# Optimization experiments

Measured on AMD Instinct MI355X. Metric: run time of the kernel, lower is better.

## Reference

```python
import jax, jax.numpy as jnp
import numpy as np

B, S, H, NH = 4, 2048, 512, 8  # batch, seq, hidden, heads
D = H // NH                    # head dim = 64


def setup_inputs() -> dict:
    key = jax.random.key(0)
    ks = jax.random.split(key, 12)
    wscale = 1.0 / np.sqrt(H)
    mk = lambda k, sh: jax.random.normal(k, sh, jnp.float32)
    return {
        "q": mk(ks[0], (B, S, H)),
        "k": mk(ks[1], (B, S, H)),
        "v": mk(ks[2], (B, S, H)),
        "k_b": mk(ks[3], (B, S, H)),
        "mask": jax.random.randint(ks[4], (B, S), 0, 2).astype(jnp.int32),
        "Wq": mk(ks[5], (H, H)) * wscale, "bq": jnp.zeros((H,), jnp.float32),
        "Wk": mk(ks[6], (H, H)) * wscale, "bk": jnp.zeros((H,), jnp.float32),
        "Wv": mk(ks[7], (H, H)) * wscale, "bv": jnp.zeros((H,), jnp.float32),
        "Wkb": mk(ks[8], (H, H)) * wscale, "bkb": jnp.zeros((H,), jnp.float32),
        "Wo": mk(ks[9], (H, H)) * wscale, "bo": jnp.zeros((H,), jnp.float32),
    }


def _attn(q, k, v, k_b, mask, Wq, bq, Wk, bk, Wv, bv, Wkb, bkb, Wo, bo):
    b, s, h = q.shape
    proj = lambda x, W, bias: (x @ W + bias).reshape(b, s, NH, D).transpose(0, 2, 1, 3)
    qh = proj(q, Wq, bq)      # [b, nh, s, d]
    kh = proj(k, Wk, bk)
    vh = proj(v, Wv, bv)
    kbh = proj(k_b, Wkb, bkb)
    # q@k^T + q@k_b^T == q@(k+k_b)^T, scaled by sqrt(d)
    corr = jnp.einsum('bhqd,bhkd->bhqk', qh, kh + kbh) / jnp.sqrt(jnp.float32(D))
    # torch mask repeat pattern depends only on key index -> broadcast over q and heads
    corr = jnp.where(mask[:, None, None, :] == 0, jnp.float32(-1e9), corr)
    prob = jax.nn.softmax(corr, axis=-1)  # dropout inactive (eval mode)
    hid = jnp.einsum('bhqk,bhkd->bhqd', prob, vh)
    hid = hid.transpose(0, 2, 1, 3).reshape(b, s, h)
    return hid @ Wo + bo


def reference(q, k, v, k_b, mask, Wq, bq, Wk, bk, Wv, bv, Wkb, bkb, Wo, bo):
    return _attn(q, k, v, k_b, mask, Wq, bq, Wk, bk, Wv, bv, Wkb, bkb, Wo, bo)
```

## Files before the change

kernel.cpp:

```cpp
#include <hip/hip_runtime.h>
#include <hip/hip_bf16.h>
#include <math.h>

#define B_  4
#define S_  2048
#define H_  512
#define NH_ 8
#define D_  64

typedef __attribute__((ext_vector_type(8))) short bf16x8;
typedef __attribute__((ext_vector_type(4))) float f32x4;
#define MFMA16(a, b, c) __builtin_amdgcn_mfma_f32_16x16x32_bf16(a, b, c, 0, 0, 0)

__device__ __forceinline__ unsigned short f2bf(float f) {
    union { float f; unsigned int i; } x; x.f = f;
    unsigned int i = x.i;
    i += 0x7fffu + ((i >> 16) & 1u);
    return (unsigned short)(i >> 16);
}
__device__ __forceinline__ unsigned int pk2(float lo, float hi) {
    union { __hip_bfloat162 h; unsigned int u; } c;
    c.h = __float22bfloat162_rn(make_float2(lo, hi));
    return c.u;
}
__device__ __forceinline__ void gl_lds16(const void* g, void* l) {
    __builtin_amdgcn_global_load_lds(
        (const __attribute__((address_space(1))) unsigned int*)g,
        (__attribute__((address_space(3))) unsigned int*)l, 16, 0, 0);
}

__global__ __launch_bounds__(256) void prep_w(
    const float* __restrict__ W0, const float* __restrict__ W1,
    const float* __restrict__ W2, const float* __restrict__ W3,
    unsigned short* __restrict__ Wt)
{
    const float* Ws[4] = {W0, W1, W2, W3};
    const float* W = Ws[blockIdx.z];
    unsigned short* Y = Wt + (size_t)blockIdx.z * H_ * H_;
    __shared__ float Tl[64][68];
    const int t = threadIdx.x;
    const int k0 = blockIdx.y * 64, n0 = blockIdx.x * 64;
    #pragma unroll
    for (int i = 0; i < 4; ++i) {
        const int e = (t + 256 * i) * 4;
        const int r = e >> 6, c = e & 63;
        const float4 a = *(const float4*)(W + (size_t)(k0 + r) * H_ + n0 + c);
        Tl[c + 0][r] = a.x; Tl[c + 1][r] = a.y;
        Tl[c + 2][r] = a.z; Tl[c + 3][r] = a.w;
    }
    __syncthreads();
    #pragma unroll
    for (int i = 0; i < 4; ++i) {
        const int e = (t + 256 * i) * 4;
        const int n = e >> 6, c = e & 63;
        uint2 p;
        p.x = pk2(Tl[n][c + 0], Tl[n][c + 1]);
        p.y = pk2(Tl[n][c + 2], Tl[n][c + 3]);
        *(uint2*)(Y + (size_t)(n0 + n) * H_ + k0 + c) = p;
    }
}

__global__ __launch_bounds__(256, 3) void proj_all(
    const float* __restrict__ q,  const float* __restrict__ k,
    const float* __restrict__ v,  const float* __restrict__ k_b,
    const unsigned short* __restrict__ Wt,
    const float* __restrict__ bq, const float* __restrict__ bk,
    const float* __restrict__ bkb,const float* __restrict__ bv,
    unsigned short* __restrict__ Qf, unsigned short* __restrict__ Kf,
    unsigned short* __restrict__ Vf)
{
    __shared__ __align__(16) unsigned short LB[17408];
    unsigned short* As = LB;
    unsigned short* Bs = LB + 8192;

    const int z = blockIdx.z;
    const float *X, *bias, *X2 = nullptr, *bias2 = nullptr;
    const unsigned short *Wa, *Wb = nullptr;
    unsigned short* Y;
    bool VT = false;
    const size_t WSZ = (size_t)H_ * H_;
    if (z == 0)      { X = q; Wa = Wt;           bias = bq; Y = Qf; }
    else if (z == 1) { X = k; Wa = Wt + WSZ;     bias = bk;
                       X2 = k_b; Wb = Wt + 2 * WSZ; bias2 = bkb; Y = Kf; }
    else             { X = v; Wa = Wt + 3 * WSZ; bias = bv; Y = Vf; VT = true; }

    const int t = threadIdx.x;
    const int w = t >> 6, lane = t & 63;
    const int quad = lane >> 4, l15 = lane & 15;
    const int wr = w >> 1, wc = w & 1;
    const int m0 = blockIdx.x * 128, n0 = blockIdx.y * 128;

    const f32x4 zero = {0.f, 0.f, 0.f, 0.f};
    f32x4 acc[4][4];
    #pragma unroll
    for (int i = 0; i < 4; ++i)
        #pragma unroll
        for (int j = 0; j < 4; ++j) acc[i][j] = zero;

    const int npass = (X2 != nullptr) ? 2 : 1;
    for (int pass = 0; pass < npass; ++pass) {
        const float* Xp = pass ? X2 : X;
        const unsigned short* Wp = pass ? Wb : Wa;
        for (int kb0 = 0; kb0 < H_; kb0 += 64) {
            __syncthreads();
            #pragma unroll
            for (int i = 0; i < 4; ++i) {
                const int c = w * 4 + i;
                const int u = c * 64 + lane;
                const int row = u >> 3;
                const int sc  = ((u & 7) ^ (row & 7)) << 3;
                gl_lds16(Wp + (size_t)(n0 + row) * H_ + kb0 + sc, Bs + c * 512);
            }
            float4 av[8];
            #pragma unroll
            for (int i = 0; i < 8; ++i) {
                const int e = (t + 256 * i) * 4;
                av[i] = *(const float4*)(Xp + (size_t)(m0 + (e >> 6)) * H_ + kb0 + (e & 63));
            }
            #pragma unroll
            for (int i = 0; i < 8; ++i) {
                const int e = (t + 256 * i) * 4;
                const int row = e >> 6, kc = e & 63;
                uint2 p; p.x = pk2(av[i].x, av[i].y); p.y = pk2(av[i].z, av[i].w);
                *(uint2*)&As[row * 64 + ((((kc >> 3) ^ (row & 7)) << 3) | (kc & 7))] = p;
            }
            __syncthreads();
            #pragma unroll
            for (int ks = 0; ks < 2; ++ks) {
                bf16x8 af[4], bfr[4];
                #pragma unroll
                for (int i = 0; i < 4; ++i) {
                    const int row = wr * 64 + i * 16 + l15;
                    af[i] = *(const bf16x8*)&As[row * 64 +
                                (((ks * 4 + quad) ^ (row & 7)) << 3)];
                }
                #pragma unroll
                for (int j = 0; j < 4; ++j) {
                    const int nrw = wc * 64 + j * 16 + l15;
                    bfr[j] = *(const bf16x8*)&Bs[nrw * 64 +
                                (((ks * 4 + quad) ^ (nrw & 7)) << 3)];
                }
                #pragma unroll
                for (int i = 0; i < 4; ++i)
                    #pragma unroll
                    for (int j = 0; j < 4; ++j)
                        acc[i][j] = MFMA16(af[i], bfr[j], acc[i][j]);
            }
        }
    }

    const int bb = m0 >> 11, s0 = m0 & (S_ - 1);
    if (!VT) {
        #pragma unroll
        for (int i = 0; i < 4; ++i)
            #pragma unroll
            for (int r = 0; r < 4; ++r) {
                const int s = s0 + wr * 64 + i * 16 + quad * 4 + r;
                #pragma unroll
                for (int j = 0; j < 4; ++j) {
                    const int nn = n0 + wc * 64 + j * 16 + l15;
                    const int h = nn >> 6, d = nn & 63;
                    float val = acc[i][j][r] + bias[nn];
                    if (bias2) val += bias2[nn];
                    Y[(((size_t)bb * NH_ + h) * S_ + s) * D_ + d] = f2bf(val);
                }
            }
    } else {
        __syncthreads();
        #pragma unroll
        for (int i = 0; i < 4; ++i)
            #pragma unroll
            for (int r = 0; r < 4; ++r) {
                const int ml = wr * 64 + i * 16 + quad * 4 + r;
                #pragma unroll
                for (int j = 0; j < 4; ++j) {
                    const int nl = wc * 64 + j * 16 + l15;
                    LB[nl * 136 + ml] = f2bf(acc[i][j][r] + bias[n0 + nl]);
                }
            }
        __syncthreads();
        const int nr = t >> 1, half = t & 1;
        const int nn = n0 + nr, h = nn >> 6, d = nn & 63;
        const size_t vbase = (((size_t)bb * NH_ + h) * D_ + d) * S_ + s0 + half * 64;
        #pragma unroll
        for (int i = 0; i < 16; ++i)
            *(ushort4*)(Y + vbase + i * 4) =
                *(const ushort4*)&LB[nr * 136 + half * 64 + i * 4];
    }
}

__global__ __launch_bounds__(256) void attn_mfma(
    unsigned short* QHd,
    const unsigned short* __restrict__ Kh, const unsigned short* __restrict__ Vt,
    const int* __restrict__ mask)
{
    const int b = blockIdx.z, h = blockIdx.y;
    const int q0 = blockIdx.x * 128;
    const int t = threadIdx.x;
    const int w = t >> 6, lane = t & 63;
    const int quad = lane >> 4, l15 = lane & 15;

    __shared__ __align__(16) unsigned short Ks[2][64][72];
    __shared__ __align__(16) unsigned short Vs[2][64][72];
    __shared__ __align__(16) unsigned short Ps[128][72];
    __shared__ int mk[2][64];

    const size_t head = ((size_t)b * NH_ + h) * S_;
    unsigned short* Qbase = QHd + head * D_;
    const unsigned short* Kbase = Kh + head * D_;
    const unsigned short* Vbase = Vt + head * D_;

    bf16x8 qf[2][2];
    #pragma unroll
    for (int rt = 0; rt < 2; ++rt)
        #pragma unroll
        for (int ds = 0; ds < 2; ++ds)
            qf[rt][ds] = *(const bf16x8*)(
                Qbase + (size_t)(q0 + w * 32 + rt * 16 + l15) * D_ + ds * 32 + quad * 8);

    const f32x4 zero = {0.f, 0.f, 0.f, 0.f};
    f32x4 O[2][4];
    #pragma unroll
    for (int rt = 0; rt < 2; ++rt)
        #pragma unroll
        for (int dt = 0; dt < 4; ++dt) O[rt][dt] = zero;
    float lsum[2][4] = {};
    const float SC2 = 0.125f * 1.44269504089f;

    #define STAGE(kt_) do {                                                        \
        const int bf_ = (kt_) & 1, k0_ = (kt_) * 64;                               \
        _Pragma("unroll")                                                          \
        for (int i_ = 0; i_ < 4; ++i_) {                                           \
            const int e_ = (t + 256 * i_) * 4;                                     \
            const int r_ = e_ >> 6, c_ = e_ & 63;                                  \
            *(ushort4*)&Ks[bf_][r_][c_] =                                          \
                *(const ushort4*)(Kbase + (size_t)(k0_ + r_) * D_ + c_);           \
            *(ushort4*)&Vs[bf_][r_][c_] =                                          \
                *(const ushort4*)(Vbase + (size_t)r_ * S_ + k0_ + c_);             \
        }                                                                          \
        if (t < 64) mk[bf_][t] = mask[b * S_ + k0_ + t];                           \
    } while (0)

    STAGE(0);
    __syncthreads();

    for (int kt = 0; kt < S_ / 64; ++kt) {
        const int bf = kt & 1;
        if (kt + 1 < S_ / 64) STAGE(kt + 1);

        float pv[2][4][4];
        #pragma unroll
        for (int ct = 0; ct < 4; ++ct) {
            const bf16x8 kf0 = *(const bf16x8*)&Ks[bf][ct * 16 + l15][quad * 8];
            const bf16x8 kf1 = *(const bf16x8*)&Ks[bf][ct * 16 + l15][32 + quad * 8];
            const float msel = (mk[bf][ct * 16 + l15] == 0) ? -1e9f : 0.f;
            #pragma unroll
            for (int rt = 0; rt < 2; ++rt) {
                f32x4 acc = zero;
                acc = MFMA16(qf[rt][0], kf0, acc);
                acc = MFMA16(qf[rt][1], kf1, acc);
                #pragma unroll
                for (int r = 0; r < 4; ++r) {
                    const float p = __builtin_amdgcn_exp2f(fmaf(acc[r], SC2, msel));
                    pv[rt][ct][r] = p;
                    lsum[rt][r] += p;
                }
            }
        }
        #pragma unroll
        for (int rt = 0; rt < 2; ++rt)
            #pragma unroll
            for (int r = 0; r < 4; ++r) {
                const int row = w * 32 + rt * 16 + quad * 4 + r;
                #pragma unroll
                for (int ct = 0; ct < 4; ++ct)
                    Ps[row][ct * 16 + l15] = f2bf(pv[rt][ct][r]);
            }
        bf16x8 pf[2][2];
        #pragma unroll
        for (int rt = 0; rt < 2; ++rt) {
            pf[rt][0] = *(const bf16x8*)&Ps[w * 32 + rt * 16 + l15][quad * 8];
            pf[rt][1] = *(const bf16x8*)&Ps[w * 32 + rt * 16 + l15][32 + quad * 8];
        }
        #pragma unroll
        for (int dt = 0; dt < 4; ++dt) {
            const bf16x8 vf0 = *(const bf16x8*)&Vs[bf][dt * 16 + l15][quad * 8];
            const bf16x8 vf1 = *(const bf16x8*)&Vs[bf][dt * 16 + l15][32 + quad * 8];
            #pragma unroll
            for (int rt = 0; rt < 2; ++rt) {
                O[rt][dt] = MFMA16(pf[rt][0], vf0, O[rt][dt]);
                O[rt][dt] = MFMA16(pf[rt][1], vf1, O[rt][dt]);
            }
        }
        __syncthreads();
    }
    #undef STAGE

    #pragma unroll
    for (int off = 1; off <= 8; off <<= 1)
        #pragma unroll
        for (int rt = 0; rt < 2; ++rt)
            #pragma unroll
            for (int r = 0; r < 4; ++r)
                lsum[rt][r] += __shfl_xor(lsum[rt][r], off, 64);
    float inv[2][4];
    #pragma unroll
    for (int rt = 0; rt < 2; ++rt)
        #pragma unroll
        for (int r = 0; r < 4; ++r) inv[rt][r] = 1.f / lsum[rt][r];
    #pragma unroll
    for (int rt = 0; rt < 2; ++rt)
        #pragma unroll
        for (int dt = 0; dt < 4; ++dt)
            #pragma unroll
            for (int r = 0; r < 4; ++r) {
                const int row = w * 32 + rt * 16 + quad * 4 + r;
                Qbase[(size_t)(q0 + row) * D_ + dt * 16 + l15] =
                    f2bf(O[rt][dt][r] * inv[rt][r]);
            }
}

__global__ __launch_bounds__(256) void out_mfma(
    const unsigned short* __restrict__ Hd, const unsigned short* __restrict__ Wot,
    const float* __restrict__ bias, float* __restrict__ Out)
{
    __shared__ __align__(16) unsigned short As[8192];
    __shared__ __align__(16) unsigned short Bs[4096];
    const int t = threadIdx.x;
    const int w = t >> 6, lane = t & 63;
    const int quad = lane >> 4, l15 = lane & 15;
    const int wr = w >> 1, wc = w & 1;
    const int m0 = blockIdx.x * 128, n0 = blockIdx.y * 64;
    const int bb = m0 >> 11, s0 = m0 & (S_ - 1);

    const f32x4 zero = {0.f, 0.f, 0.f, 0.f};
    f32x4 acc[4][2];
    #pragma unroll
    for (int i = 0; i < 4; ++i)
        #pragma unroll
        for (int j = 0; j < 2; ++j) acc[i][j] = zero;

    for (int kb0 = 0; kb0 < H_; kb0 += 64) {
        const int hk = kb0 >> 6;
        const unsigned short* Ab = Hd + (((size_t)bb * NH_ + hk) * S_ + s0) * D_;
        __syncthreads();
        #pragma unroll
        for (int i = 0; i < 4; ++i) {
            const int c = w * 4 + i, u = c * 64 + lane, row = u >> 3;
            const int sc = ((u & 7) ^ (row & 7)) << 3;
            gl_lds16(Ab + (size_t)row * D_ + sc, As + c * 512);
        }
        #pragma unroll
        for (int i = 0; i < 2; ++i) {
            const int c = w * 2 + i, u = c * 64 + lane, row = u >> 3;
            const int sc = ((u & 7) ^ (row & 7)) << 3;
            gl_lds16(Wot + (size_t)(n0 + row) * H_ + kb0 + sc, Bs + c * 512);
        }
        __syncthreads();
        #pragma unroll
        for (int ks = 0; ks < 2; ++ks) {
            bf16x8 af[4], bfr[2];
            #pragma unroll
            for (int i = 0; i < 4; ++i) {
                const int row = wr * 64 + i * 16 + l15;
                af[i] = *(const bf16x8*)&As[row * 64 +
                            (((ks * 4 + quad) ^ (row & 7)) << 3)];
            }
            #pragma unroll
            for (int j = 0; j < 2; ++j) {
                const int nrw = wc * 32 + j * 16 + l15;
                bfr[j] = *(const bf16x8*)&Bs[nrw * 64 +
                            (((ks * 4 + quad) ^ (nrw & 7)) << 3)];
            }
            #pragma unroll
            for (int i = 0; i < 4; ++i)
                #pragma unroll
                for (int j = 0; j < 2; ++j)
                    acc[i][j] = MFMA16(af[i], bfr[j], acc[i][j]);
        }
    }
    #pragma unroll
    for (int i = 0; i < 4; ++i)
        #pragma unroll
        for (int r = 0; r < 4; ++r) {
            const int m = m0 + wr * 64 + i * 16 + quad * 4 + r;
            #pragma unroll
            for (int j = 0; j < 2; ++j) {
                const int n = n0 + wc * 32 + j * 16 + l15;
                Out[(size_t)m * H_ + n] = acc[i][j][r] + bias[n];
            }
        }
}

__global__ void fill_kernel(float* __restrict__ out, float val, int n) {
    const int i = blockIdx.x * 256 + threadIdx.x;
    if (i < n) out[i] = val;
}

extern "C" void kernel_launch(void* const* d_in, const int* in_sizes, int n_in,
                              void* d_out, int out_size, void* d_ws, size_t ws_size,
                              hipStream_t stream) {
    const float* q   = (const float*)d_in[0];
    const float* k   = (const float*)d_in[1];
    const float* v   = (const float*)d_in[2];
    const float* k_b = (const float*)d_in[3];
    const int*   msk = (const int*)d_in[4];
    const float* Wq  = (const float*)d_in[5];
    const float* bq  = (const float*)d_in[6];
    const float* Wk  = (const float*)d_in[7];
    const float* bk  = (const float*)d_in[8];
    const float* Wv  = (const float*)d_in[9];
    const float* bv  = (const float*)d_in[10];
    const float* Wkb = (const float*)d_in[11];
    const float* bkb = (const float*)d_in[12];
    const float* Wo  = (const float*)d_in[13];
    const float* bo  = (const float*)d_in[14];
    float* out = (float*)d_out;

    const size_t PER  = (size_t)B_ * NH_ * S_ * D_;
    const size_t NEED = 3 * PER * sizeof(unsigned short);
    if (ws_size < NEED) {
        fill_kernel<<<(out_size + 255) / 256, 256, 0, stream>>>(
            out, (float)((ws_size >> 20) + 2), out_size);
        return;
    }
    unsigned short* wsh = (unsigned short*)d_ws;
    unsigned short* Qf  = wsh;
    unsigned short* Kf  = wsh + PER;
    unsigned short* Vf  = wsh + 2 * PER;

    unsigned short* Wt = (unsigned short*)d_out;

    dim3 gw(8, 8, 4);
    prep_w<<<gw, 256, 0, stream>>>(Wq, Wk, Wkb, Wv, Wt);

    dim3 gp((B_ * S_) / 128, H_ / 128, 3);
    proj_all<<<gp, 256, 0, stream>>>(q, k, v, k_b, Wt, bq, bk, bkb, bv, Qf, Kf, Vf);

    dim3 ga(S_ / 128, NH_, B_);
    attn_mfma<<<ga, 256, 0, stream>>>(Qf, Kf, Vf, msk);

    dim3 gw1(8, 8, 1);
    prep_w<<<gw1, 256, 0, stream>>>(Wo, Wo, Wo, Wo, Kf);

    dim3 go((B_ * S_) / 128, H_ / 64, 1);
    out_mfma<<<go, 256, 0, stream>>>(Qf, Kf, bo, out);
}
```

Baseline: 243.4 us.

## Swizzle LDS tiles, use direct global-to-LDS loads, transpose QK MFMA in attention

The attention kernel replaces padded K/V/P shared-memory tiles with XOR-swizzled unpadded layouts. K and V tiles are now staged with direct global-to-LDS 16-byte loads through a gl_lds16 helper. The QK^T MFMA is computed transposed (K as the A operand), so each lane holds four consecutive key columns of one query row. That lets P be written as packed bf16 pairs and keeps the row-sum per lane, needing only two cross-quad shuffles. The mask is converted once per block into a float bias array in LDS, which removes the per-tile mask staging. The larger mask buffer raises LDS use, and correctness depends on the swizzle and the helper being consistent.

```diff
diff --git a/kernel.cpp b/kernel.cpp
--- a/kernel.cpp
+++ b/kernel.cpp
@@ -200,16 +200,19 @@
     const int w = t >> 6, lane = t & 63;
     const int quad = lane >> 4, l15 = lane & 15;
 
-    __shared__ __align__(16) unsigned short Ks[2][64][72];
-    __shared__ __align__(16) unsigned short Vs[2][64][72];
-    __shared__ __align__(16) unsigned short Ps[128][72];
-    __shared__ int mk[2][64];
+    __shared__ __align__(16) unsigned short KsL[2 * 4096];
+    __shared__ __align__(16) unsigned short VsL[2 * 4096];
+    __shared__ __align__(16) unsigned short Ps[128 * 64];
+    __shared__ float mskf[S_];
 
     const size_t head = ((size_t)b * NH_ + h) * S_;
     unsigned short* Qbase = QHd + head * D_;
     const unsigned short* Kbase = Kh + head * D_;
     const unsigned short* Vbase = Vt + head * D_;
 
+    for (int i = t; i < S_; i += 256)
+        mskf[i] = (mask[b * S_ + i] == 0) ? -1e9f : 0.f;
+
     bf16x8 qf[2][2];
     #pragma unroll
     for (int rt = 0; rt < 2; ++rt)
@@ -224,21 +227,22 @@
     for (int rt = 0; rt < 2; ++rt)
         #pragma unroll
         for (int dt = 0; dt < 4; ++dt) O[rt][dt] = zero;
-    float lsum[2][4] = {};
+    float lsum[2] = {0.f, 0.f};
     const float SC2 = 0.125f * 1.44269504089f;
 
     #define STAGE(kt_) do {                                                        \
         const int bf_ = (kt_) & 1, k0_ = (kt_) * 64;                               \
         _Pragma("unroll")                                                          \
-        for (int i_ = 0; i_ < 4; ++i_) {                                           \
-            const int e_ = (t + 256 * i_) * 4;                                     \
-            const int r_ = e_ >> 6, c_ = e_ & 63;                                  \
-            *(ushort4*)&Ks[bf_][r_][c_] =                                          \
-                *(const ushort4*)(Kbase + (size_t)(k0_ + r_) * D_ + c_);           \
-            *(ushort4*)&Vs[bf_][r_][c_] =                                          \
-                *(const ushort4*)(Vbase + (size_t)r_ * S_ + k0_ + c_);             \
+        for (int i_ = 0; i_ < 2; ++i_) {                                           \
+            const int c_ = w * 2 + i_;                                             \
+            const int u_ = c_ * 64 + lane;                                         \
+            const int row_ = u_ >> 3;                                              \
+            const int sc_ = ((u_ & 7) ^ (row_ & 7)) << 3;                          \
+            gl_lds16(Kbase + (size_t)(k0_ + row_) * D_ + sc_,                      \
+                     KsL + bf_ * 4096 + c_ * 512);                                 \
+            gl_lds16(Vbase + (size_t)row_ * S_ + k0_ + sc_,                        \
+                     VsL + bf_ * 4096 + c_ * 512);                                 \
         }                                                                          \
-        if (t < 64) mk[bf_][t] = mask[b * S_ + k0_ + t];                           \
     } while (0)
 
     STAGE(0);
@@ -246,46 +250,46 @@
 
     for (int kt = 0; kt < S_ / 64; ++kt) {
         const int bf = kt & 1;
+        const int k0 = kt * 64;
         if (kt + 1 < S_ / 64) STAGE(kt + 1);
 
-        float pv[2][4][4];
         #pragma unroll
         for (int ct = 0; ct < 4; ++ct) {
-            const bf16x8 kf0 = *(const bf16x8*)&Ks[bf][ct * 16 + l15][quad * 8];
-            const bf16x8 kf1 = *(const bf16x8*)&Ks[bf][ct * 16 + l15][32 + quad * 8];
-            const float msel = (mk[bf][ct * 16 + l15] == 0) ? -1e9f : 0.f;
+            const int krow = ct * 16 + l15;
+            const unsigned short* Kb = KsL + bf * 4096 + krow * 64;
+            const bf16x8 kf0 = *(const bf16x8*)&Kb[(quad ^ (krow & 7)) << 3];
+            const bf16x8 kf1 = *(const bf16x8*)&Kb[((4 + quad) ^ (krow & 7)) << 3];
+            const float4 ms4 = *(const float4*)&mskf[k0 + ct * 16 + quad * 4];
             #pragma unroll
             for (int rt = 0; rt < 2; ++rt) {
                 f32x4 acc = zero;
-                acc = MFMA16(qf[rt][0], kf0, acc);
-                acc = MFMA16(qf[rt][1], kf1, acc);
-                #pragma unroll
-                for (int r = 0; r < 4; ++r) {
-                    const float p = __builtin_amdgcn_exp2f(fmaf(acc[r], SC2, msel));
-                    pv[rt][ct][r] = p;
-                    lsum[rt][r] += p;
-                }
-            }
-        }
-        #pragma unroll
-        for (int rt = 0; rt < 2; ++rt)
-            #pragma unroll
-            for (int r = 0; r < 4; ++r) {
-                const int row = w * 32 + rt * 16 + quad * 4 + r;
-                #pragma unroll
-                for (int ct = 0; ct < 4; ++ct)
-                    Ps[row][ct * 16 + l15] = f2bf(pv[rt][ct][r]);
-            }
+                acc = MFMA16(kf0, qf[rt][0], acc);
+                acc = MFMA16(kf1, qf[rt][1], acc);
+                float pr[4];
+                pr[0] = __builtin_amdgcn_exp2f(fmaf(acc[0], SC2, ms4.x));
+                pr[1] = __builtin_amdgcn_exp2f(fmaf(acc[1], SC2, ms4.y));
+                pr[2] = __builtin_amdgcn_exp2f(fmaf(acc[2], SC2, ms4.z));
+                pr[3] = __builtin_amdgcn_exp2f(fmaf(acc[3], SC2, ms4.w));
+                lsum[rt] += (pr[0] + pr[1]) + (pr[2] + pr[3]);
+                uint2 pw; pw.x = pk2(pr[0], pr[1]); pw.y = pk2(pr[2], pr[3]);
+                const int prow = w * 32 + rt * 16 + l15;
+                const int unit = (ct * 2 + (quad >> 1)) ^ (prow & 7);
+                *(uint2*)&Ps[prow * 64 + unit * 8 + (quad & 1) * 4] = pw;
+            }
+        }
         bf16x8 pf[2][2];
         #pragma unroll
         for (int rt = 0; rt < 2; ++rt) {
-            pf[rt][0] = *(const bf16x8*)&Ps[w * 32 + rt * 16 + l15][quad * 8];
-            pf[rt][1] = *(const bf16x8*)&Ps[w * 32 + rt * 16 + l15][32 + quad * 8];
+            const int prow = w * 32 + rt * 16 + l15;
+            pf[rt][0] = *(const bf16x8*)&Ps[prow * 64 + ((quad ^ (prow & 7)) << 3)];
+            pf[rt][1] = *(const bf16x8*)&Ps[prow * 64 + (((4 + quad) ^ (prow & 7)) << 3)];
         }
         #pragma unroll
         for (int dt = 0; dt < 4; ++dt) {
-            const bf16x8 vf0 = *(const bf16x8*)&Vs[bf][dt * 16 + l15][quad * 8];
-            const bf16x8 vf1 = *(const bf16x8*)&Vs[bf][dt * 16 + l15][32 + quad * 8];
+            const int vrow = dt * 16 + l15;
+            const unsigned short* Vb = VsL + bf * 4096 + vrow * 64;
+            const bf16x8 vf0 = *(const bf16x8*)&Vb[(quad ^ (vrow & 7)) << 3];
+            const bf16x8 vf1 = *(const bf16x8*)&Vb[((4 + quad) ^ (vrow & 7)) << 3];
             #pragma unroll
             for (int rt = 0; rt < 2; ++rt) {
                 O[rt][dt] = MFMA16(pf[rt][0], vf0, O[rt][dt]);
@@ -297,17 +301,16 @@
     #undef STAGE
 
     #pragma unroll
-    for (int off = 1; off <= 8; off <<= 1)
-        #pragma unroll
-        for (int rt = 0; rt < 2; ++rt)
-            #pragma unroll
-            for (int r = 0; r < 4; ++r)
-                lsum[rt][r] += __shfl_xor(lsum[rt][r], off, 64);
+    for (int rt = 0; rt < 2; ++rt) {
+        lsum[rt] += __shfl_xor(lsum[rt], 16, 64);
+        lsum[rt] += __shfl_xor(lsum[rt], 32, 64);
+    }
     float inv[2][4];
     #pragma unroll
     for (int rt = 0; rt < 2; ++rt)
         #pragma unroll
-        for (int r = 0; r < 4; ++r) inv[rt][r] = 1.f / lsum[rt][r];
+        for (int r = 0; r < 4; ++r)
+            inv[rt][r] = 1.f / __shfl(lsum[rt], quad * 4 + r, 64);
     #pragma unroll
     for (int rt = 0; rt < 2; ++rt)
         #pragma unroll
```

New measurement: 242.2 us. Within noise of the previous version (-0.5%).
